# Kernel tuning notes

Hardware: AMD Instinct MI355X
Metric: run time of the kernel (lower is better)

The kernel has to match this reference:

```python
import jax, jax.numpy as jnp
import numpy as np

WINDOW_SIZES = (2, 4, 8)
HIDDEN = 32


def setup_inputs() -> dict:
    key = jax.random.key(0)
    ks = jax.random.split(key, 8)
    B, H, L = 4, 16, 1024
    S = len(WINDOW_SIZES)
    inp = {
        "attn_1": jax.random.uniform(ks[0], (B, H, L, L), dtype=jnp.float32),
        "attn_2": jax.random.uniform(ks[1], (B, H, L, L), dtype=jnp.float32),
        # gate MLP params, stacked over scales: Linear(8->32), Linear(32->16), Linear(16->1)
        "W1": jax.random.normal(ks[2], (S, HIDDEN, 8), dtype=jnp.float32) * 0.2,
        "b1": jnp.zeros((S, HIDDEN), dtype=jnp.float32),
        "W2": jax.random.normal(ks[3], (S, HIDDEN // 2, HIDDEN), dtype=jnp.float32) * 0.2,
        "b2": jnp.zeros((S, HIDDEN // 2), dtype=jnp.float32),
        "W3": jax.random.normal(ks[4], (S, 1, HIDDEN // 2), dtype=jnp.float32) * 0.2,
        "b3": jnp.zeros((S, 1), dtype=jnp.float32),
        "scale_weights": jnp.ones((S,), dtype=jnp.float32) / S,
    }
    return inp


def _window_stats(attn, ws):
    # attn: [B,H,L,L]; L % ws == 0 -> all windows are full-size (no edge merge)
    B, H, L, _ = attn.shape
    nw = L // ws
    x = attn.reshape(B, H, nw, ws, L)
    mean = x.mean(axis=-1).mean(axis=-1)                 # [B,H,nw]
    std = jnp.std(x, axis=-1, ddof=1).mean(axis=-1)      # torch.std is unbiased
    mx = x.max(axis=-1).mean(axis=-1)
    mn = x.min(axis=-1).mean(axis=-1)
    return jnp.stack([mean, std, mx, mn], axis=-1)        # [B,H,nw,4]


def reference(attn_1, attn_2, W1, b1, W2, b2, W3, b3, scale_weights):
    B, H, L, _ = attn_1.shape
    alphas = []
    for s, ws in enumerate(WINDOW_SIZES):
        g = jnp.concatenate([_window_stats(attn_1, ws), _window_stats(attn_2, ws)], axis=-1)  # [B,H,nw,8]
        h = jax.nn.relu(jnp.einsum('bhnf,of->bhno', g, W1[s]) + b1[s])
        h = jax.nn.relu(jnp.einsum('bhnf,of->bhno', h, W2[s]) + b2[s])
        a = jax.nn.sigmoid(jnp.einsum('bhnf,of->bhno', h, W3[s]) + b3[s])  # [B,H,nw,1]
        # expand per-window alpha to per-frame: repeat ws times (nw*ws == L)
        a_exp = jnp.repeat(a[..., 0], ws, axis=-1)[..., None]  # [B,H,L,1]
        alphas.append(a_exp)
    w = jax.nn.softmax(scale_weights)                     # all scales valid (max ws <= L)
    alpha_stacked = jnp.stack(alphas, axis=-1)            # [B,H,L,1,S]
    alpha_final = (alpha_stacked * w.reshape(1, 1, 1, 1, -1)).sum(axis=-1)
    return alpha_final
```

## Files before the change

kernel.cpp:

```cpp
#include <hip/hip_runtime.h>
#include <math.h>

#define L_DIM 1024
#define BH 64
#define ROWS_PER_TENSOR (BH * L_DIM)

__global__ __launch_bounds__(256) void row_stats_kernel(
    const float* __restrict__ a1, const float* __restrict__ a2,
    float4* __restrict__ stats)
{
    const int wave = (blockIdx.x << 2) | (threadIdx.x >> 6);
    const int lane = threadIdx.x & 63;
    const int t = wave >> 16;
    const int r = wave & (ROWS_PER_TENSOR - 1);
    const float* __restrict__ src = t ? a2 : a1;
    const float4* __restrict__ rowp = (const float4*)(src + (size_t)r * L_DIM);

    float s = 0.f, sq = 0.f, mx = -INFINITY, mn = INFINITY;
#pragma unroll
    for (int c = 0; c < 4; ++c) {
        float4 v = rowp[(c << 6) + lane];
        s  += v.x + v.y + v.z + v.w;
        sq += v.x * v.x + v.y * v.y + v.z * v.z + v.w * v.w;
        mx = fmaxf(mx, fmaxf(fmaxf(v.x, v.y), fmaxf(v.z, v.w)));
        mn = fminf(mn, fminf(fminf(v.x, v.y), fminf(v.z, v.w)));
    }
#pragma unroll
    for (int off = 32; off > 0; off >>= 1) {
        s  += __shfl_xor(s,  off, 64);
        sq += __shfl_xor(sq, off, 64);
        mx = fmaxf(mx, __shfl_xor(mx, off, 64));
        mn = fminf(mn, __shfl_xor(mn, off, 64));
    }
    if (lane == 0) {
        const float invL = 1.0f / (float)L_DIM;
        float mean = s * invL;
        float var  = (sq - s * s * invL) * (1.0f / (float)(L_DIM - 1));
        var = fmaxf(var, 0.f);
        float4 o;
        o.x = mean; o.y = sqrtf(var); o.z = mx; o.w = mn;
        stats[wave] = o;
    }
}

#define NW_TOTAL 896

__global__ __launch_bounds__(256) void gate_kernel(
    const float4* __restrict__ stats,
    const float* __restrict__ W1, const float* __restrict__ b1,
    const float* __restrict__ W2, const float* __restrict__ b2,
    const float* __restrict__ W3, const float* __restrict__ b3,
    const float* __restrict__ sw,
    float* __restrict__ out)
{
    __shared__ float wts[2499];
    __shared__ float alpha[NW_TOTAL];

    for (int i = threadIdx.x; i < 2499; i += 256) {
        float v;
        if (i < 768)        v = W1[i];
        else if (i < 864)   v = b1[i - 768];
        else if (i < 2400)  v = W2[i - 864];
        else if (i < 2448)  v = b2[i - 2400];
        else if (i < 2496)  v = W3[i - 2448];
        else                v = b3[i - 2496];
        wts[i] = v;
    }
    __syncthreads();

    const int bh = blockIdx.x;
    const float4* __restrict__ st1 = stats + (size_t)bh * L_DIM;
    const float4* __restrict__ st2 = stats + ROWS_PER_TENSOR + (size_t)bh * L_DIM;

    for (int idx = threadIdx.x; idx < NW_TOTAL; idx += 256) {
        int s, w, ws, aoff;
        if (idx < 512)       { s = 0; w = idx;       ws = 2; aoff = 0;   }
        else if (idx < 768)  { s = 1; w = idx - 512; ws = 4; aoff = 512; }
        else                 { s = 2; w = idx - 768; ws = 8; aoff = 768; }

        float g[8] = {0.f, 0.f, 0.f, 0.f, 0.f, 0.f, 0.f, 0.f};
        const int r0 = w * ws;
        for (int j = 0; j < ws; ++j) {
            float4 v1 = st1[r0 + j];
            float4 v2 = st2[r0 + j];
            g[0] += v1.x; g[1] += v1.y; g[2] += v1.z; g[3] += v1.w;
            g[4] += v2.x; g[5] += v2.y; g[6] += v2.z; g[7] += v2.w;
        }
        const float inv = 1.0f / (float)ws;
#pragma unroll
        for (int k = 0; k < 8; ++k) g[k] *= inv;

        float h1[32];
        const float* W1p = wts + s * 256;
        const float* b1p = wts + 768 + s * 32;
#pragma unroll
        for (int o = 0; o < 32; ++o) {
            float acc = b1p[o];
#pragma unroll
            for (int f = 0; f < 8; ++f) acc += W1p[o * 8 + f] * g[f];
            h1[o] = fmaxf(acc, 0.f);
        }
        float h2[16];
        const float* W2p = wts + 864 + s * 512;
        const float* b2p = wts + 2400 + s * 16;
#pragma unroll
        for (int o = 0; o < 16; ++o) {
            float acc = b2p[o];
#pragma unroll
            for (int f = 0; f < 32; ++f) acc += W2p[o * 32 + f] * h1[f];
            h2[o] = fmaxf(acc, 0.f);
        }
        const float* W3p = wts + 2448 + s * 16;
        float acc = wts[2496 + s];
#pragma unroll
        for (int f = 0; f < 16; ++f) acc += W3p[f] * h2[f];
        alpha[aoff + w] = 1.0f / (1.0f + expf(-acc));
    }
    __syncthreads();

    const float s0 = sw[0], s1 = sw[1], s2 = sw[2];
    const float m = fmaxf(s0, fmaxf(s1, s2));
    const float e0 = expf(s0 - m), e1 = expf(s1 - m), e2 = expf(s2 - m);
    const float einv = 1.0f / (e0 + e1 + e2);
    const float w0 = e0 * einv, w1 = e1 * einv, w2 = e2 * einv;

    float* __restrict__ outp = out + (size_t)bh * L_DIM;
    for (int l = threadIdx.x; l < L_DIM; l += 256) {
        outp[l] = w0 * alpha[l >> 1]
                + w1 * alpha[512 + (l >> 2)]
                + w2 * alpha[768 + (l >> 3)];
    }
}

extern "C" void kernel_launch(void* const* d_in, const int* in_sizes, int n_in,
                              void* d_out, int out_size, void* d_ws, size_t ws_size,
                              hipStream_t stream) {
    const float* attn1 = (const float*)d_in[0];
    const float* attn2 = (const float*)d_in[1];
    const float* W1 = (const float*)d_in[2];
    const float* b1 = (const float*)d_in[3];
    const float* W2 = (const float*)d_in[4];
    const float* b2 = (const float*)d_in[5];
    const float* W3 = (const float*)d_in[6];
    const float* b3 = (const float*)d_in[7];
    const float* sw = (const float*)d_in[8];
    float* out = (float*)d_out;

    float4* stats = (float4*)d_ws;

    const int n_rows = 2 * ROWS_PER_TENSOR;
    row_stats_kernel<<<n_rows / 4, 256, 0, stream>>>(attn1, attn2, stats);

    gate_kernel<<<BH, 256, 0, stream>>>(stats, W1, b1, W2, b2, W3, b3, sw, out);
}
```

Before: 530.0 us.

## Use nontemporal loads for row stats and split gate kernel across more blocks

```diff
diff --git a/kernel.cpp b/kernel.cpp
--- a/kernel.cpp
+++ b/kernel.cpp
@@ -4,6 +4,8 @@
 #define L_DIM 1024
 #define BH 64
 #define ROWS_PER_TENSOR (BH * L_DIM)
+
+typedef float floatx4 __attribute__((ext_vector_type(4)));
 
 __global__ __launch_bounds__(256) void row_stats_kernel(
     const float* __restrict__ a1, const float* __restrict__ a2,
@@ -14,12 +16,12 @@
     const int t = wave >> 16;
     const int r = wave & (ROWS_PER_TENSOR - 1);
     const float* __restrict__ src = t ? a2 : a1;
-    const float4* __restrict__ rowp = (const float4*)(src + (size_t)r * L_DIM);
+    const floatx4* __restrict__ rowp = (const floatx4*)(src + (size_t)r * L_DIM);
 
     float s = 0.f, sq = 0.f, mx = -INFINITY, mn = INFINITY;
 #pragma unroll
     for (int c = 0; c < 4; ++c) {
-        float4 v = rowp[(c << 6) + lane];
+        floatx4 v = __builtin_nontemporal_load(&rowp[(c << 6) + lane]);
         s  += v.x + v.y + v.z + v.w;
         sq += v.x * v.x + v.y * v.y + v.z * v.z + v.w * v.w;
         mx = fmaxf(mx, fmaxf(fmaxf(v.x, v.y), fmaxf(v.z, v.w)));
@@ -43,8 +45,6 @@
     }
 }
 
-#define NW_TOTAL 896
-
 __global__ __launch_bounds__(256) void gate_kernel(
     const float4* __restrict__ stats,
     const float* __restrict__ W1, const float* __restrict__ b1,
@@ -53,33 +53,30 @@
     const float* __restrict__ sw,
     float* __restrict__ out)
 {
-    __shared__ float wts[2499];
-    __shared__ float alpha[NW_TOTAL];
+    __shared__ float alpha[224];
 
-    for (int i = threadIdx.x; i < 2499; i += 256) {
-        float v;
-        if (i < 768)        v = W1[i];
-        else if (i < 864)   v = b1[i - 768];
-        else if (i < 2400)  v = W2[i - 864];
-        else if (i < 2448)  v = b2[i - 2400];
-        else if (i < 2496)  v = W3[i - 2448];
-        else                v = b3[i - 2496];
-        wts[i] = v;
-    }
-    __syncthreads();
+    const int bh = blockIdx.x >> 2;
+    const int l0 = (blockIdx.x & 3) << 8;
+    const int tid = threadIdx.x;
 
-    const int bh = blockIdx.x;
     const float4* __restrict__ st1 = stats + (size_t)bh * L_DIM;
     const float4* __restrict__ st2 = stats + ROWS_PER_TENSOR + (size_t)bh * L_DIM;
 
-    for (int idx = threadIdx.x; idx < NW_TOTAL; idx += 256) {
-        int s, w, ws, aoff;
-        if (idx < 512)       { s = 0; w = idx;       ws = 2; aoff = 0;   }
-        else if (idx < 768)  { s = 1; w = idx - 512; ws = 4; aoff = 512; }
-        else                 { s = 2; w = idx - 768; ws = 8; aoff = 768; }
+    if (tid < 224) {
+        int s, ws, r0;
+        if (tid < 128)      { s = 0; ws = 2; r0 = l0 + (tid << 1); }
+        else if (tid < 192) { s = 1; ws = 4; r0 = l0 + ((tid - 128) << 2); }
+        else                { s = 2; ws = 8; r0 = l0 + ((tid - 192) << 3); }
+
+        const int su = __builtin_amdgcn_readfirstlane(s);
+        const float* __restrict__ W1p = W1 + su * 256;
+        const float* __restrict__ b1p = b1 + su * 32;
+        const float* __restrict__ W2p = W2 + su * 512;
+        const float* __restrict__ b2p = b2 + su * 16;
+        const float* __restrict__ W3p = W3 + su * 16;
+        const float  b3v = b3[su];
 
         float g[8] = {0.f, 0.f, 0.f, 0.f, 0.f, 0.f, 0.f, 0.f};
-        const int r0 = w * ws;
         for (int j = 0; j < ws; ++j) {
             float4 v1 = st1[r0 + j];
             float4 v2 = st2[r0 + j];
@@ -91,8 +88,6 @@
         for (int k = 0; k < 8; ++k) g[k] *= inv;
 
         float h1[32];
-        const float* W1p = wts + s * 256;
-        const float* b1p = wts + 768 + s * 32;
 #pragma unroll
         for (int o = 0; o < 32; ++o) {
             float acc = b1p[o];
@@ -101,8 +96,6 @@
             h1[o] = fmaxf(acc, 0.f);
         }
         float h2[16];
-        const float* W2p = wts + 864 + s * 512;
-        const float* b2p = wts + 2400 + s * 16;
 #pragma unroll
         for (int o = 0; o < 16; ++o) {
             float acc = b2p[o];
@@ -110,11 +103,11 @@
             for (int f = 0; f < 32; ++f) acc += W2p[o * 32 + f] * h1[f];
             h2[o] = fmaxf(acc, 0.f);
         }
-        const float* W3p = wts + 2448 + s * 16;
-        float acc = wts[2496 + s];
+        float acc = b3v;
 #pragma unroll
         for (int f = 0; f < 16; ++f) acc += W3p[f] * h2[f];
-        alpha[aoff + w] = 1.0f / (1.0f + expf(-acc));
+
+        alpha[tid] = 1.0f / (1.0f + expf(-acc));
     }
     __syncthreads();
 
@@ -124,12 +117,10 @@
     const float einv = 1.0f / (e0 + e1 + e2);
     const float w0 = e0 * einv, w1 = e1 * einv, w2 = e2 * einv;
 
-    float* __restrict__ outp = out + (size_t)bh * L_DIM;
-    for (int l = threadIdx.x; l < L_DIM; l += 256) {
-        outp[l] = w0 * alpha[l >> 1]
-                + w1 * alpha[512 + (l >> 2)]
-                + w2 * alpha[768 + (l >> 3)];
-    }
+    out[(size_t)bh * L_DIM + l0 + tid] =
+          w0 * alpha[tid >> 1]
+        + w1 * alpha[128 + (tid >> 2)]
+        + w2 * alpha[192 + (tid >> 3)];
 }
 
 extern "C" void kernel_launch(void* const* d_in, const int* in_sizes, int n_in,
@@ -151,5 +142,5 @@
     const int n_rows = 2 * ROWS_PER_TENSOR;
     row_stats_kernel<<<n_rows / 4, 256, 0, stream>>>(attn1, attn2, stats);
 
-    gate_kernel<<<BH, 256, 0, stream>>>(stats, W1, b1, W2, b2, W3, b3, sw, out);
+    gate_kernel<<<BH * 4, 256, 0, stream>>>(stats, W1, b1, W2, b2, W3, b3, sw, out);
 }
```

Result: faster. 497.7 us (-6.1%).
